# Optimization experiments

Hardware: AMD Instinct MI355X
Metric: run time of the kernel (lower is better)

## Reference

```python
import jax, jax.numpy as jnp
import numpy as np

IN_C, OUT_C, MAX_SIZE = 512, 256, 256
N = MAX_SIZE * MAX_SIZE  # 65536 nodes
E = MAX_SIZE * MAX_SIZE  # 65536 edges (before self loops)
NEG_SLOPE = 0.2


def setup_inputs() -> dict:
    key = jax.random.key(0)
    ks = jax.random.split(key, 12)
    s = 1.0 / np.sqrt(IN_C)
    so = 1.0 / np.sqrt(OUT_C)
    return {
        "x": jax.random.normal(ks[0], (N, IN_C), dtype=jnp.float32),
        "x_mask": jnp.ones((N,), dtype=bool),
        "edge_index": jax.random.randint(ks[1], (2, E), 0, N),
        "edge_mask": jnp.ones((E,), dtype=bool),
        "vaild_mask": jnp.ones((MAX_SIZE, MAX_SIZE), dtype=bool),
        # self-loop Linear
        "W_self": jax.random.uniform(ks[2], (IN_C, OUT_C), jnp.float32, -s, s),
        "b_self": jax.random.uniform(ks[3], (OUT_C,), jnp.float32, -s, s),
        # GATv2Conv params (heads=1)
        "W_l": jax.random.uniform(ks[4], (IN_C, OUT_C), jnp.float32, -s, s),
        "b_l": jnp.zeros((OUT_C,), jnp.float32),
        "W_r": jax.random.uniform(ks[5], (IN_C, OUT_C), jnp.float32, -s, s),
        "b_r": jnp.zeros((OUT_C,), jnp.float32),
        "att": jax.random.uniform(ks[6], (OUT_C,), jnp.float32, -so, so),
        "conv_bias": jnp.zeros((OUT_C,), jnp.float32),
        # sk classifier (out_channels -> 1)
        "W_cls": jax.random.uniform(ks[7], (OUT_C, 1), jnp.float32, -so, so),
        "b_cls": jax.random.uniform(ks[8], (1,), jnp.float32, -so, so),
    }


def _forward(x, edge_index, W_self, b_self, W_l, b_l, W_r, b_r, att,
             conv_bias, W_cls, b_cls):
    n = x.shape[0]
    # PyG GATv2Conv adds self-loops by default
    loops = jnp.arange(n, dtype=edge_index.dtype)
    src = jnp.concatenate([edge_index[0], loops])
    dst = jnp.concatenate([edge_index[1], loops])

    x_l = x @ W_l + b_l  # source-side transform (n, out)
    x_r = x @ W_r + b_r  # target-side transform (n, out)

    # per-edge GATv2 attention logits
    h = jax.nn.leaky_relu(x_l[src] + x_r[dst], NEG_SLOPE)  # (Etot, out)
    e = h @ att  # (Etot,)

    # segment softmax over incoming edges of each target node
    m = jnp.full((n,), -jnp.inf, dtype=e.dtype).at[dst].max(e)
    p = jnp.exp(e - m[dst])
    denom = jax.ops.segment_sum(p, dst, num_segments=n)
    alpha = p / denom[dst]

    x_neigh = jax.ops.segment_sum(alpha[:, None] * x_l[src], dst,
                                  num_segments=n) + conv_bias
    x_out = (x @ W_self + b_self) + x_neigh

    # sinkhorn-style row softmax channel (sk_channel=1, n1=n2=max_size)
    ms = MAX_SIZE
    sk = (x_out @ W_cls + b_cls).reshape(ms, ms)
    sk = jax.nn.softmax(sk, axis=-1)
    x_out = x_out + sk.reshape(-1, 1)
    # n1*n2 == max_size**2, so the padded output equals x_out
    return x_out


def reference(x, x_mask, edge_index, edge_mask, vaild_mask, W_self, b_self,
              W_l, b_l, W_r, b_r, att, conv_bias, W_cls, b_cls):
    # masks are all-True (fully valid case): x_valid = x, edges all kept
    return _forward(x, edge_index, W_self, b_self, W_l, b_l, W_r, b_r, att,
                    conv_bias, W_cls, b_cls)
```

## Files before the change

kernel.cpp:

```cpp
#include <hip/hip_runtime.h>
#include <hip/hip_bf16.h>
#include <stdint.h>

#define NNODE 65536
#define NEDGE 65536
#define ETOT  (NNODE + NEDGE)
#define INC   512
#define OUTC  256
#define NEG_SLOPE 0.2f
#define SLOTCAP 32

typedef __attribute__((ext_vector_type(8))) __bf16 bf16x8;
typedef __attribute__((ext_vector_type(4))) float f32x4;

__device__ __forceinline__ float b2f(unsigned short u) {
  return __uint_as_float(((unsigned int)u) << 16);
}
__device__ __forceinline__ unsigned short f2b(float f) {
  unsigned int u = __float_as_uint(f);
  u += 0x7fffu + ((u >> 16) & 1u);
  return (unsigned short)(u >> 16);
}
__device__ __forceinline__ unsigned int pk2(float lo, float hi) {
  return (unsigned int)f2b(lo) | ((unsigned int)f2b(hi) << 16);
}
__device__ __forceinline__ float lrelu(float v) {
  return v > 0.f ? v : NEG_SLOPE * v;
}

__global__ __launch_bounds__(256) void cvt_x_kernel(const float* __restrict__ x,
                                                    unsigned short* __restrict__ xb,
                                                    int* __restrict__ cnt) {
  if (blockIdx.x < 256) cnt[blockIdx.x * 256 + threadIdx.x] = 0;
  size_t i = ((size_t)blockIdx.x * 256 + threadIdx.x) * 8;
  float4 v0 = *(const float4*)(x + i);
  float4 v1 = *(const float4*)(x + i + 4);
  uint4 o;
  o.x = pk2(v0.x, v0.y);
  o.y = pk2(v0.z, v0.w);
  o.z = pk2(v1.x, v1.y);
  o.w = pk2(v1.z, v1.w);
  *(uint4*)(xb + i) = o;
}

__global__ __launch_bounds__(256) void prep_w_kernel(
    const float* __restrict__ Wl, const float* __restrict__ Wr, const float* __restrict__ Ws,
    const float* __restrict__ bl, const float* __restrict__ br, const float* __restrict__ bs,
    unsigned short* __restrict__ WT, float* __restrict__ bcat) {
  int i = blockIdx.x * 256 + threadIdx.x;
  if (i < 768 * 512) {
    int o = i >> 9, k = i & 511;
    float v;
    if (o < 256)      v = Wl[k * 256 + o];
    else if (o < 512) v = Wr[k * 256 + (o - 256)];
    else              v = Ws[k * 256 + (o - 512)];
    WT[i] = f2b(v);
  }
  if (i < 768) {
    bcat[i] = (i < 256) ? bl[i] : (i < 512 ? br[i - 256] : bs[i - 512]);
  }
}

__global__ __launch_bounds__(512) void gemm_kernel(
    const unsigned short* __restrict__ Xb,
    const unsigned short* __restrict__ WT,
    const float* __restrict__ bcat,
    const float* __restrict__ Wcls,
    unsigned short* __restrict__ xl,
    unsigned short* __restrict__ xr,
    unsigned short* __restrict__ xs,
    float* __restrict__ g,
    float* __restrict__ gs) {
  __shared__ __align__(16) char smem[98304];
  unsigned short* ring = (unsigned short*)smem;

  const int wid = blockIdx.x;
  const int xcd = wid & 7;
  const int local = wid >> 3;
  const int by = local % 3;
  const int rowt = xcd * 32 + local / 3;
  const int rowBase = rowt * 256;
  const int colBase = by * 256;

  const int tid = threadIdx.x;
  const int lane = tid & 63;
  const int w = tid >> 6;
  const int wm = (w >> 2) * 128;
  const int wn = (w & 3) * 64;

  f32x4 acc[8][4] = {};

  auto stageh = [&](int c, int hf) {
    const int kk = c * 32;
    const int buf = c % 3;
    const int q = tid;
    const int sl = q & 3;
    const unsigned short* basep = hf ? (WT + (size_t)colBase * 512) : (Xb + (size_t)rowBase * 512);
    unsigned short* ldst = ring + buf * 16384 + hf * 8192;
#pragma unroll
    for (int l = 0; l < 2; ++l) {
      const int r = l * 128 + (q >> 2);
      const int slot = sl ^ ((r >> 1) & 3);
      const unsigned short* gp = basep + (size_t)r * 512 + kk + slot * 8;
      __builtin_amdgcn_global_load_lds(
          (const __attribute__((address_space(1))) void*)gp,
          (__attribute__((address_space(3))) void*)(ldst + l * 4096 + q * 8), 16, 0, 0);
    }
  };

  stageh(0, 0); stageh(0, 1);
  stageh(1, 0); stageh(1, 1);
  asm volatile("s_waitcnt vmcnt(4)" ::: "memory");
  __builtin_amdgcn_s_barrier();

#pragma unroll
  for (int c = 0; c < 16; ++c) {
    const unsigned short* As = ring + (c % 3) * 16384;
    const unsigned short* Bs = As + 8192;
    const int kq = lane >> 4;
    bf16x8 fa[8], fb[4];

#pragma unroll
    for (int m = 0; m < 4; ++m) {
      const int rA = wm + m * 16 + (lane & 15);
      fa[m] = *(const bf16x8*)&As[rA * 32 + ((kq ^ ((rA >> 1) & 3)) << 3)];
    }
#pragma unroll
    for (int n = 0; n < 4; ++n) {
      const int rB = wn + n * 16 + (lane & 15);
      fb[n] = *(const bf16x8*)&Bs[rB * 32 + ((kq ^ ((rB >> 1) & 3)) << 3)];
    }
    if (c + 2 < 16) stageh(c + 2, 0);
    __builtin_amdgcn_s_barrier();
    asm volatile("s_waitcnt lgkmcnt(0)" ::: "memory");
    __builtin_amdgcn_sched_barrier(0);
    __builtin_amdgcn_s_setprio(1);
#pragma unroll
    for (int m = 0; m < 4; ++m)
#pragma unroll
      for (int n = 0; n < 4; ++n)
        acc[m][n] = __builtin_amdgcn_mfma_f32_16x16x32_bf16(fa[m], fb[n], acc[m][n], 0, 0, 0);
    __builtin_amdgcn_s_setprio(0);
    __builtin_amdgcn_s_barrier();

#pragma unroll
    for (int m = 4; m < 8; ++m) {
      const int rA = wm + m * 16 + (lane & 15);
      fa[m] = *(const bf16x8*)&As[rA * 32 + ((kq ^ ((rA >> 1) & 3)) << 3)];
    }
    if (c + 2 < 16) stageh(c + 2, 1);
    __builtin_amdgcn_s_barrier();
    asm volatile("s_waitcnt lgkmcnt(0)" ::: "memory");
    __builtin_amdgcn_sched_barrier(0);
    __builtin_amdgcn_s_setprio(1);
#pragma unroll
    for (int m = 4; m < 8; ++m)
#pragma unroll
      for (int n = 0; n < 4; ++n)
        acc[m][n] = __builtin_amdgcn_mfma_f32_16x16x32_bf16(fa[m], fb[n], acc[m][n], 0, 0, 0);
    __builtin_amdgcn_s_setprio(0);
    if (c <= 13)      asm volatile("s_waitcnt vmcnt(4)" ::: "memory");
    else if (c == 14) asm volatile("s_waitcnt vmcnt(0)" ::: "memory");
    __builtin_amdgcn_s_barrier();
  }

  {
    unsigned short* dst = (by == 0) ? xl : (by == 1) ? xr : xs;
    const bool doG = (by != 1);
    float* eps = (float*)smem + w * 1088;
    float* gpart = (float*)(smem + 40960);
    float biasn[4], wcn[4];
#pragma unroll
    for (int n = 0; n < 4; ++n) {
      biasn[n] = bcat[colBase + wn + n * 16 + (lane & 15)];
      wcn[n] = Wcls[wn + n * 16 + (lane & 15)];
    }
#pragma unroll
    for (int m = 0; m < 8; ++m) {
      float rp[4] = {0.f, 0.f, 0.f, 0.f};
#pragma unroll
      for (int n = 0; n < 4; ++n)
#pragma unroll
        for (int j = 0; j < 4; ++j) {
          const float v = acc[m][n][j] + biasn[n];
          eps[((lane >> 4) * 4 + j) * 68 + n * 16 + (lane & 15)] = v;
          rp[j] += v * wcn[n];
        }
#pragma unroll
      for (int it = 0; it < 2; ++it) {
        const int r16 = it * 8 + (lane >> 3);
        const int c8 = (lane & 7) * 8;
        const float* srcp = eps + r16 * 68 + c8;
        float4 v0 = *(const float4*)srcp;
        float4 v1 = *(const float4*)(srcp + 4);
        uint4 o;
        o.x = pk2(v0.x, v0.y);
        o.y = pk2(v0.z, v0.w);
        o.z = pk2(v1.x, v1.y);
        o.w = pk2(v1.z, v1.w);
        *(uint4*)(dst + (size_t)(rowBase + wm + m * 16 + r16) * 256 + wn + c8) = o;
      }
      if (doG) {
#pragma unroll
        for (int j = 0; j < 4; ++j) {
          float s = rp[j];
          s += __shfl_xor(s, 1);
          s += __shfl_xor(s, 2);
          s += __shfl_xor(s, 4);
          s += __shfl_xor(s, 8);
          if ((lane & 15) == 0)
            gpart[(wm + m * 16 + (lane >> 4) * 4 + j) * 4 + (w & 3)] = s;
        }
      }
    }
    __syncthreads();
    if (doG && tid < 256) {
      float s = gpart[tid * 4] + gpart[tid * 4 + 1] + gpart[tid * 4 + 2] + gpart[tid * 4 + 3];
      ((by == 0) ? g : gs)[rowBase + tid] = s;
    }
  }
}

__global__ __launch_bounds__(256) void edge_logit_kernel(
    const int* __restrict__ ei,
    const unsigned short* __restrict__ xl,
    const unsigned short* __restrict__ xr,
    const float* __restrict__ att,
    int* __restrict__ cnt,
    int* __restrict__ slot_src,
    float* __restrict__ slot_e) {
  const int j = blockIdx.x * 8 + (threadIdx.x >> 5);
  const int lane = threadIdx.x & 31;
  int src, dst;
  if (j < NEDGE) { src = ei[j]; dst = ei[NEDGE + j]; }
  else           { src = j - NEDGE; dst = src; }
  const int c = lane * 8;
  uint4 ul = *(const uint4*)(xl + (size_t)src * 256 + c);
  uint4 ur = *(const uint4*)(xr + (size_t)dst * 256 + c);
  float4 a0 = *(const float4*)(att + c);
  float4 a1 = *(const float4*)(att + c + 4);
  float s = lrelu(b2f((unsigned short)ul.x) + b2f((unsigned short)ur.x)) * a0.x
          + lrelu(b2f((unsigned short)(ul.x >> 16)) + b2f((unsigned short)(ur.x >> 16))) * a0.y
          + lrelu(b2f((unsigned short)ul.y) + b2f((unsigned short)ur.y)) * a0.z
          + lrelu(b2f((unsigned short)(ul.y >> 16)) + b2f((unsigned short)(ur.y >> 16))) * a0.w
          + lrelu(b2f((unsigned short)ul.z) + b2f((unsigned short)ur.z)) * a1.x
          + lrelu(b2f((unsigned short)(ul.z >> 16)) + b2f((unsigned short)(ur.z >> 16))) * a1.y
          + lrelu(b2f((unsigned short)ul.w) + b2f((unsigned short)ur.w)) * a1.z
          + lrelu(b2f((unsigned short)(ul.w >> 16)) + b2f((unsigned short)(ur.w >> 16))) * a1.w;
#pragma unroll
  for (int off = 16; off; off >>= 1) s += __shfl_xor(s, off);
  if (lane == 0) {
    const int pos = atomicAdd(&cnt[dst], 1);
    if (pos < SLOTCAP) {
      slot_src[dst * SLOTCAP + pos] = src;
      slot_e[dst * SLOTCAP + pos] = s;
    }
  }
}

__global__ __launch_bounds__(256) void logit_kernel(
    const int* __restrict__ cnt,
    const int* __restrict__ slot_src, const float* __restrict__ slot_e,
    const float* __restrict__ g, const float* __restrict__ gs,
    float* __restrict__ logits) {
  const int n = blockIdx.x * 256 + threadIdx.x;
  const int base = n * SLOTCAP;
  const int deg = cnt[n];
  float m = -1e30f;
  for (int k = 0; k < deg; ++k) m = fmaxf(m, slot_e[base + k]);
  float denom = 0.f, wsum = 0.f;
  for (int k = 0; k < deg; ++k) {
    const float p = __expf(slot_e[base + k] - m);
    denom += p;
    wsum += p * g[slot_src[base + k]];
  }
  logits[n] = gs[n] + wsum / denom;
}

__global__ __launch_bounds__(256) void node_sk_kernel(
    const int* __restrict__ cnt,
    const int* __restrict__ slot_src, const float* __restrict__ slot_e,
    const unsigned short* __restrict__ xl,
    const unsigned short* __restrict__ xs,
    const float* __restrict__ conv_bias,
    const float* __restrict__ logits,
    float* __restrict__ out) {
  const int n = blockIdx.x * 4 + (threadIdx.x >> 6);
  const int lane = threadIdx.x & 63;
  const int base = n * SLOTCAP;
  const int deg = cnt[n];

  float m = -1e30f;
  for (int k = 0; k < deg; ++k) m = fmaxf(m, slot_e[base + k]);
  float denom = 0.f;
  for (int k = 0; k < deg; ++k) denom += __expf(slot_e[base + k] - m);
  const float inv = 1.f / denom;

  const int c = lane * 4;
  float4 accv = {0.f, 0.f, 0.f, 0.f};
  for (int k = 0; k < deg; ++k) {
    const float alpha = __expf(slot_e[base + k] - m) * inv;
    const int src = slot_src[base + k];
    ushort4 u = *(const ushort4*)(xl + (size_t)src * 256 + c);
    accv.x += alpha * b2f(u.x);
    accv.y += alpha * b2f(u.y);
    accv.z += alpha * b2f(u.z);
    accv.w += alpha * b2f(u.w);
  }

  const int r = n >> 8;
  float4 lv = *(const float4*)(logits + r * 256 + c);
  float lm = fmaxf(fmaxf(lv.x, lv.y), fmaxf(lv.z, lv.w));
#pragma unroll
  for (int off = 32; off; off >>= 1) lm = fmaxf(lm, __shfl_xor(lm, off));
  float ls = __expf(lv.x - lm) + __expf(lv.y - lm) + __expf(lv.z - lm) + __expf(lv.w - lm);
#pragma unroll
  for (int off = 32; off; off >>= 1) ls += __shfl_xor(ls, off);
  const float softval = __expf(logits[n] - lm) / ls;

  ushort4 s4 = *(const ushort4*)(xs + (size_t)n * 256 + c);
  float4 cb = *(const float4*)(conv_bias + c);
  float4 cur;
  cur.x = b2f(s4.x) + accv.x + cb.x + softval;
  cur.y = b2f(s4.y) + accv.y + cb.y + softval;
  cur.z = b2f(s4.z) + accv.z + cb.z + softval;
  cur.w = b2f(s4.w) + accv.w + cb.w + softval;
  *(float4*)(out + (size_t)n * 256 + c) = cur;
}

extern "C" void kernel_launch(void* const* d_in, const int* in_sizes, int n_in,
                              void* d_out, int out_size, void* d_ws, size_t ws_size,
                              hipStream_t stream) {
  const float* x        = (const float*)d_in[0];
  const int*   ei       = (const int*)d_in[2];
  const float* W_self   = (const float*)d_in[5];
  const float* b_self   = (const float*)d_in[6];
  const float* W_l      = (const float*)d_in[7];
  const float* b_l      = (const float*)d_in[8];
  const float* W_r      = (const float*)d_in[9];
  const float* b_r      = (const float*)d_in[10];
  const float* att      = (const float*)d_in[11];
  const float* conv_bias= (const float*)d_in[12];
  const float* W_cls    = (const float*)d_in[13];
  float* out = (float*)d_out;

  char* ws = (char*)d_ws;
  size_t off = 0;
  auto alloc = [&](size_t bytes) {
    char* p = ws + off;
    off += (bytes + 255) & ~(size_t)255;
    return p;
  };
  unsigned short* xb   = (unsigned short*)alloc((size_t)NNODE * INC * 2);
  unsigned short* WT   = (unsigned short*)alloc((size_t)768 * 512 * 2);
  float*          bcat = (float*)alloc(768 * 4);
  unsigned short* xlb  = (unsigned short*)alloc((size_t)NNODE * OUTC * 2);
  unsigned short* xrb  = (unsigned short*)alloc((size_t)NNODE * OUTC * 2);
  unsigned short* xsb  = (unsigned short*)alloc((size_t)NNODE * OUTC * 2);
  int*            cnt  = (int*)alloc((size_t)NNODE * 4);
  float*          logits  = (float*)alloc((size_t)NNODE * 4);
  float*          gbuf    = (float*)alloc((size_t)NNODE * 4);
  float*          gsbuf   = (float*)alloc((size_t)NNODE * 4);
  int*   slot_src = (int*)xb;
  float* slot_e   = (float*)(xb + (size_t)NNODE * SLOTCAP * 2);
  (void)ws_size; (void)in_sizes; (void)n_in; (void)out_size;

  cvt_x_kernel<<<(NNODE * INC) / (256 * 8), 256, 0, stream>>>(x, xb, cnt);
  prep_w_kernel<<<(768 * 512 + 255) / 256, 256, 0, stream>>>(W_l, W_r, W_self, b_l, b_r, b_self, WT, bcat);
  gemm_kernel<<<768, 512, 0, stream>>>(xb, WT, bcat, W_cls, xlb, xrb, xsb, gbuf, gsbuf);
  edge_logit_kernel<<<ETOT / 8, 256, 0, stream>>>(ei, xlb, xrb, att, cnt, slot_src, slot_e);
  logit_kernel<<<NNODE / 256, 256, 0, stream>>>(cnt, slot_src, slot_e, gbuf, gsbuf, logits);
  node_sk_kernel<<<NNODE / 4, 256, 0, stream>>>(cnt, slot_src, slot_e, xlb, xsb, conv_bias,
                                                logits, out);
}
```

Before: 191.0 us.

## Fuse fp32-to-bf16 conversion of x into GEMM LDS staging

Removes the separate x conversion kernel and has the GEMM stream fp32 x into LDS, converting to bf16 while building MFMA fragments. The counter zeroing moves into the weight prep kernel, and slot buffers get their own workspace. The aim is to avoid writing and re-reading a bf16 copy of x and to drop one launch. In exchange, the GEMM reads twice as many bytes of x per column tile, uses more LDS, and adds conversion ALU work in its inner loop.

```diff
diff --git a/kernel.cpp b/kernel.cpp
--- a/kernel.cpp
+++ b/kernel.cpp
@@ -28,25 +28,10 @@
   return v > 0.f ? v : NEG_SLOPE * v;
 }
 
-__global__ __launch_bounds__(256) void cvt_x_kernel(const float* __restrict__ x,
-                                                    unsigned short* __restrict__ xb,
-                                                    int* __restrict__ cnt) {
-  if (blockIdx.x < 256) cnt[blockIdx.x * 256 + threadIdx.x] = 0;
-  size_t i = ((size_t)blockIdx.x * 256 + threadIdx.x) * 8;
-  float4 v0 = *(const float4*)(x + i);
-  float4 v1 = *(const float4*)(x + i + 4);
-  uint4 o;
-  o.x = pk2(v0.x, v0.y);
-  o.y = pk2(v0.z, v0.w);
-  o.z = pk2(v1.x, v1.y);
-  o.w = pk2(v1.z, v1.w);
-  *(uint4*)(xb + i) = o;
-}
-
 __global__ __launch_bounds__(256) void prep_w_kernel(
     const float* __restrict__ Wl, const float* __restrict__ Wr, const float* __restrict__ Ws,
     const float* __restrict__ bl, const float* __restrict__ br, const float* __restrict__ bs,
-    unsigned short* __restrict__ WT, float* __restrict__ bcat) {
+    unsigned short* __restrict__ WT, float* __restrict__ bcat, int* __restrict__ cnt) {
   int i = blockIdx.x * 256 + threadIdx.x;
   if (i < 768 * 512) {
     int o = i >> 9, k = i & 511;
@@ -56,13 +41,14 @@
     else              v = Ws[k * 256 + (o - 512)];
     WT[i] = f2b(v);
   }
+  if (i < NNODE) cnt[i] = 0;
   if (i < 768) {
     bcat[i] = (i < 256) ? bl[i] : (i < 512 ? br[i - 256] : bs[i - 512]);
   }
 }
 
 __global__ __launch_bounds__(512) void gemm_kernel(
-    const unsigned short* __restrict__ Xb,
+    const float* __restrict__ Xf,
     const unsigned short* __restrict__ WT,
     const float* __restrict__ bcat,
     const float* __restrict__ Wcls,
@@ -71,8 +57,7 @@
     unsigned short* __restrict__ xs,
     float* __restrict__ g,
     float* __restrict__ gs) {
-  __shared__ __align__(16) char smem[98304];
-  unsigned short* ring = (unsigned short*)smem;
+  __shared__ __align__(16) char smem[147456];
 
   const int wid = blockIdx.x;
   const int xcd = wid & 7;
@@ -90,47 +75,67 @@
 
   f32x4 acc[8][4] = {};
 
-  auto stageh = [&](int c, int hf) {
+  auto stageA = [&](int c) {
     const int kk = c * 32;
-    const int buf = c % 3;
+    float* abase = (float*)(smem + (c % 3) * 49152);
+    const int q = tid;
+#pragma unroll
+    for (int l = 0; l < 4; ++l) {
+      const int r = l * 64 + (q >> 3);
+      const int slot = (q & 7) ^ (r & 7);
+      const float* gp = Xf + (size_t)(rowBase + r) * 512 + kk + slot * 4;
+      __builtin_amdgcn_global_load_lds(
+          (const __attribute__((address_space(1))) void*)gp,
+          (__attribute__((address_space(3))) void*)(abase + l * 2048 + q * 4), 16, 0, 0);
+    }
+  };
+  auto stageB = [&](int c) {
+    const int kk = c * 32;
+    unsigned short* bbase = (unsigned short*)(smem + (c % 3) * 49152 + 32768);
     const int q = tid;
     const int sl = q & 3;
-    const unsigned short* basep = hf ? (WT + (size_t)colBase * 512) : (Xb + (size_t)rowBase * 512);
-    unsigned short* ldst = ring + buf * 16384 + hf * 8192;
 #pragma unroll
     for (int l = 0; l < 2; ++l) {
       const int r = l * 128 + (q >> 2);
       const int slot = sl ^ ((r >> 1) & 3);
-      const unsigned short* gp = basep + (size_t)r * 512 + kk + slot * 8;
+      const unsigned short* gp = WT + (size_t)(colBase + r) * 512 + kk + slot * 8;
       __builtin_amdgcn_global_load_lds(
           (const __attribute__((address_space(1))) void*)gp,
-          (__attribute__((address_space(3))) void*)(ldst + l * 4096 + q * 8), 16, 0, 0);
+          (__attribute__((address_space(3))) void*)(bbase + l * 4096 + q * 8), 16, 0, 0);
     }
   };
 
-  stageh(0, 0); stageh(0, 1);
-  stageh(1, 0); stageh(1, 1);
-  asm volatile("s_waitcnt vmcnt(4)" ::: "memory");
+  stageA(0); stageB(0);
+  stageA(1); stageB(1);
+  asm volatile("s_waitcnt vmcnt(6)" ::: "memory");
   __builtin_amdgcn_s_barrier();
 
 #pragma unroll
   for (int c = 0; c < 16; ++c) {
-    const unsigned short* As = ring + (c % 3) * 16384;
-    const unsigned short* Bs = As + 8192;
+    const float* Af = (const float*)(smem + (c % 3) * 49152);
+    const unsigned short* Bs = (const unsigned short*)(smem + (c % 3) * 49152 + 32768);
     const int kq = lane >> 4;
     bf16x8 fa[8], fb[4];
 
-#pragma unroll
-    for (int m = 0; m < 4; ++m) {
-      const int rA = wm + m * 16 + (lane & 15);
-      fa[m] = *(const bf16x8*)&As[rA * 32 + ((kq ^ ((rA >> 1) & 3)) << 3)];
-    }
+#define LDA(mi) { \
+      const int rA = wm + (mi) * 16 + (lane & 15); \
+      const int s0 = (2 * kq) ^ (rA & 7); \
+      const int s1 = (2 * kq + 1) ^ (rA & 7); \
+      float4 v0 = *(const float4*)&Af[rA * 32 + s0 * 4]; \
+      float4 v1 = *(const float4*)&Af[rA * 32 + s1 * 4]; \
+      union { uint4 u; bf16x8 v; } cv; \
+      cv.u.x = pk2(v0.x, v0.y); cv.u.y = pk2(v0.z, v0.w); \
+      cv.u.z = pk2(v1.x, v1.y); cv.u.w = pk2(v1.z, v1.w); \
+      fa[mi] = cv.v; \
+    }
+
+    LDA(0) LDA(1) LDA(2) LDA(3)
 #pragma unroll
     for (int n = 0; n < 4; ++n) {
       const int rB = wn + n * 16 + (lane & 15);
       fb[n] = *(const bf16x8*)&Bs[rB * 32 + ((kq ^ ((rB >> 1) & 3)) << 3)];
     }
-    if (c + 2 < 16) stageh(c + 2, 0);
+    if (c + 2 < 16) stageA(c + 2);
     __builtin_amdgcn_s_barrier();
     asm volatile("s_waitcnt lgkmcnt(0)" ::: "memory");
     __builtin_amdgcn_sched_barrier(0);
@@ -143,12 +148,9 @@
     __builtin_amdgcn_s_setprio(0);
     __builtin_amdgcn_s_barrier();
 
-#pragma unroll
-    for (int m = 4; m < 8; ++m) {
-      const int rA = wm + m * 16 + (lane & 15);
-      fa[m] = *(const bf16x8*)&As[rA * 32 + ((kq ^ ((rA >> 1) & 3)) << 3)];
-    }
-    if (c + 2 < 16) stageh(c + 2, 1);
+    LDA(4) LDA(5) LDA(6) LDA(7)
+#undef LDA
+    if (c + 2 < 16) stageB(c + 2);
     __builtin_amdgcn_s_barrier();
     asm volatile("s_waitcnt lgkmcnt(0)" ::: "memory");
     __builtin_amdgcn_sched_barrier(0);
@@ -159,7 +161,7 @@
       for (int n = 0; n < 4; ++n)
         acc[m][n] = __builtin_amdgcn_mfma_f32_16x16x32_bf16(fa[m], fb[n], acc[m][n], 0, 0, 0);
     __builtin_amdgcn_s_setprio(0);
-    if (c <= 13)      asm volatile("s_waitcnt vmcnt(4)" ::: "memory");
+    if (c <= 13)      asm volatile("s_waitcnt vmcnt(6)" ::: "memory");
     else if (c == 14) asm volatile("s_waitcnt vmcnt(0)" ::: "memory");
     __builtin_amdgcn_s_barrier();
   }
@@ -351,7 +353,6 @@
     off += (bytes + 255) & ~(size_t)255;
     return p;
   };
-  unsigned short* xb   = (unsigned short*)alloc((size_t)NNODE * INC * 2);
   unsigned short* WT   = (unsigned short*)alloc((size_t)768 * 512 * 2);
   float*          bcat = (float*)alloc(768 * 4);
   unsigned short* xlb  = (unsigned short*)alloc((size_t)NNODE * OUTC * 2);
@@ -361,13 +362,13 @@
   float*          logits  = (float*)alloc((size_t)NNODE * 4);
   float*          gbuf    = (float*)alloc((size_t)NNODE * 4);
   float*          gsbuf   = (float*)alloc((size_t)NNODE * 4);
-  int*   slot_src = (int*)xb;
-  float* slot_e   = (float*)(xb + (size_t)NNODE * SLOTCAP * 2);
+  int*   slot_src = (int*)alloc((size_t)NNODE * SLOTCAP * 4);
+  float* slot_e   = (float*)alloc((size_t)NNODE * SLOTCAP * 4);
   (void)ws_size; (void)in_sizes; (void)n_in; (void)out_size;
 
-  cvt_x_kernel<<<(NNODE * INC) / (256 * 8), 256, 0, stream>>>(x, xb, cnt);
-  prep_w_kernel<<<(768 * 512 + 255) / 256, 256, 0, stream>>>(W_l, W_r, W_self, b_l, b_r, b_self, WT, bcat);
-  gemm_kernel<<<768, 512, 0, stream>>>(xb, WT, bcat, W_cls, xlb, xrb, xsb, gbuf, gsbuf);
+  prep_w_kernel<<<(768 * 512 + 255) / 256, 256, 0, stream>>>(W_l, W_r, W_self, b_l, b_r, b_self,
+                                                             WT, bcat, cnt);
+  gemm_kernel<<<768, 512, 0, stream>>>(x, WT, bcat, W_cls, xlb, xrb, xsb, gbuf, gsbuf);
   edge_logit_kernel<<<ETOT / 8, 256, 0, stream>>>(ei, xlb, xrb, att, cnt, slot_src, slot_e);
   logit_kernel<<<NNODE / 256, 256, 0, stream>>>(cnt, slot_src, slot_e, gbuf, gsbuf, logits);
   node_sk_kernel<<<NNODE / 4, 256, 0, stream>>>(cnt, slot_src, slot_e, xlb, xsb, conv_bias,
```

Result: slower. 223.0 us (+16.7%).

## Merge prep kernels and switch GEMM to double-buffered LDS pipeline

Applied to the files above, without the earlier changes.

Fuses the x-conversion and weight-transpose kernels into one launch to save a kernel launch. The GEMM drops its 3-stage ring and split half-step schedule in favour of a simpler 2-buffer scheme: it prefetches the next k-chunk, then does all 8x4 MFMAs per step with a full vmcnt(0) wait and a barrier. LDS use falls from 96KB to 64KB and launch_bounds asks for more occupancy. The cost is less latency hiding per block, since every iteration waits for its global loads to finish.

```diff
diff --git a/kernel.cpp b/kernel.cpp
--- a/kernel.cpp
+++ b/kernel.cpp
@@ -28,11 +28,13 @@
   return v > 0.f ? v : NEG_SLOPE * v;
 }
 
-__global__ __launch_bounds__(256) void cvt_x_kernel(const float* __restrict__ x,
-                                                    unsigned short* __restrict__ xb,
-                                                    int* __restrict__ cnt) {
-  if (blockIdx.x < 256) cnt[blockIdx.x * 256 + threadIdx.x] = 0;
-  size_t i = ((size_t)blockIdx.x * 256 + threadIdx.x) * 8;
+__global__ __launch_bounds__(256) void prep_kernel(
+    const float* __restrict__ x, unsigned short* __restrict__ xb, int* __restrict__ cnt,
+    const float* __restrict__ Wl, const float* __restrict__ Wr, const float* __restrict__ Ws,
+    const float* __restrict__ bl, const float* __restrict__ br, const float* __restrict__ bs,
+    unsigned short* __restrict__ WT, float* __restrict__ bcat) {
+  const int b = blockIdx.x, t = threadIdx.x;
+  size_t i = ((size_t)b * 256 + t) * 8;
   float4 v0 = *(const float4*)(x + i);
   float4 v1 = *(const float4*)(x + i + 4);
   uint4 o;
@@ -41,27 +43,22 @@
   o.z = pk2(v1.x, v1.y);
   o.w = pk2(v1.z, v1.w);
   *(uint4*)(xb + i) = o;
-}
-
-__global__ __launch_bounds__(256) void prep_w_kernel(
-    const float* __restrict__ Wl, const float* __restrict__ Wr, const float* __restrict__ Ws,
-    const float* __restrict__ bl, const float* __restrict__ br, const float* __restrict__ bs,
-    unsigned short* __restrict__ WT, float* __restrict__ bcat) {
-  int i = blockIdx.x * 256 + threadIdx.x;
-  if (i < 768 * 512) {
-    int o = i >> 9, k = i & 511;
+  if (b < 256) cnt[b * 256 + t] = 0;
+  const int wi = b * 256 + t;
+  if (wi < 768 * 512) {
+    const int oc = wi >> 9, k = wi & 511;
     float v;
-    if (o < 256)      v = Wl[k * 256 + o];
-    else if (o < 512) v = Wr[k * 256 + (o - 256)];
-    else              v = Ws[k * 256 + (o - 512)];
-    WT[i] = f2b(v);
-  }
-  if (i < 768) {
-    bcat[i] = (i < 256) ? bl[i] : (i < 512 ? br[i - 256] : bs[i - 512]);
-  }
-}
-
-__global__ __launch_bounds__(512) void gemm_kernel(
+    if (oc < 256)      v = Wl[k * 256 + oc];
+    else if (oc < 512) v = Wr[k * 256 + (oc - 256)];
+    else               v = Ws[k * 256 + (oc - 512)];
+    WT[wi] = f2b(v);
+  }
+  if (wi < 768) {
+    bcat[wi] = (wi < 256) ? bl[wi] : (wi < 512 ? br[wi - 256] : bs[wi - 512]);
+  }
+}
+
+__global__ __launch_bounds__(512, 4) void gemm_kernel(
     const unsigned short* __restrict__ Xb,
     const unsigned short* __restrict__ WT,
     const float* __restrict__ bcat,
@@ -71,7 +68,7 @@
     unsigned short* __restrict__ xs,
     float* __restrict__ g,
     float* __restrict__ gs) {
-  __shared__ __align__(16) char smem[98304];
+  __shared__ __align__(16) char smem[65536];
   unsigned short* ring = (unsigned short*)smem;
 
   const int wid = blockIdx.x;
@@ -92,7 +89,7 @@
 
   auto stageh = [&](int c, int hf) {
     const int kk = c * 32;
-    const int buf = c % 3;
+    const int buf = c & 1;
     const int q = tid;
     const int sl = q & 3;
     const unsigned short* basep = hf ? (WT + (size_t)colBase * 512) : (Xb + (size_t)rowBase * 512);
@@ -109,19 +106,21 @@
   };
 
   stageh(0, 0); stageh(0, 1);
-  stageh(1, 0); stageh(1, 1);
-  asm volatile("s_waitcnt vmcnt(4)" ::: "memory");
+  asm volatile("s_waitcnt vmcnt(0)" ::: "memory");
   __builtin_amdgcn_s_barrier();
+  __builtin_amdgcn_sched_barrier(0);
 
 #pragma unroll
   for (int c = 0; c < 16; ++c) {
-    const unsigned short* As = ring + (c % 3) * 16384;
+    const unsigned short* As = ring + (c & 1) * 16384;
     const unsigned short* Bs = As + 8192;
     const int kq = lane >> 4;
     bf16x8 fa[8], fb[4];
 
-#pragma unroll
-    for (int m = 0; m < 4; ++m) {
+    if (c + 1 < 16) { stageh(c + 1, 0); stageh(c + 1, 1); }
+
+#pragma unroll
+    for (int m = 0; m < 8; ++m) {
       const int rA = wm + m * 16 + (lane & 15);
       fa[m] = *(const bf16x8*)&As[rA * 32 + ((kq ^ ((rA >> 1) & 3)) << 3)];
     }
@@ -130,38 +129,18 @@
       const int rB = wn + n * 16 + (lane & 15);
       fb[n] = *(const bf16x8*)&Bs[rB * 32 + ((kq ^ ((rB >> 1) & 3)) << 3)];
     }
-    if (c + 2 < 16) stageh(c + 2, 0);
-    __builtin_amdgcn_s_barrier();
     asm volatile("s_waitcnt lgkmcnt(0)" ::: "memory");
     __builtin_amdgcn_sched_barrier(0);
     __builtin_amdgcn_s_setprio(1);
 #pragma unroll
-    for (int m = 0; m < 4; ++m)
+    for (int m = 0; m < 8; ++m)
 #pragma unroll
       for (int n = 0; n < 4; ++n)
         acc[m][n] = __builtin_amdgcn_mfma_f32_16x16x32_bf16(fa[m], fb[n], acc[m][n], 0, 0, 0);
     __builtin_amdgcn_s_setprio(0);
+    asm volatile("s_waitcnt vmcnt(0)" ::: "memory");
     __builtin_amdgcn_s_barrier();
-
-#pragma unroll
-    for (int m = 4; m < 8; ++m) {
-      const int rA = wm + m * 16 + (lane & 15);
-      fa[m] = *(const bf16x8*)&As[rA * 32 + ((kq ^ ((rA >> 1) & 3)) << 3)];
-    }
-    if (c + 2 < 16) stageh(c + 2, 1);
-    __builtin_amdgcn_s_barrier();
-    asm volatile("s_waitcnt lgkmcnt(0)" ::: "memory");
     __builtin_amdgcn_sched_barrier(0);
-    __builtin_amdgcn_s_setprio(1);
-#pragma unroll
-    for (int m = 4; m < 8; ++m)
-#pragma unroll
-      for (int n = 0; n < 4; ++n)
-        acc[m][n] = __builtin_amdgcn_mfma_f32_16x16x32_bf16(fa[m], fb[n], acc[m][n], 0, 0, 0);
-    __builtin_amdgcn_s_setprio(0);
-    if (c <= 13)      asm volatile("s_waitcnt vmcnt(4)" ::: "memory");
-    else if (c == 14) asm volatile("s_waitcnt vmcnt(0)" ::: "memory");
-    __builtin_amdgcn_s_barrier();
   }
 
   {
@@ -365,8 +344,9 @@
   float* slot_e   = (float*)(xb + (size_t)NNODE * SLOTCAP * 2);
   (void)ws_size; (void)in_sizes; (void)n_in; (void)out_size;
 
-  cvt_x_kernel<<<(NNODE * INC) / (256 * 8), 256, 0, stream>>>(x, xb, cnt);
-  prep_w_kernel<<<(768 * 512 + 255) / 256, 256, 0, stream>>>(W_l, W_r, W_self, b_l, b_r, b_self, WT, bcat);
+  prep_kernel<<<(NNODE * INC) / (256 * 8), 256, 0, stream>>>(x, xb, cnt,
+                                                             W_l, W_r, W_self, b_l, b_r, b_self,
+                                                             WT, bcat);
   gemm_kernel<<<768, 512, 0, stream>>>(xb, WT, bcat, W_cls, xlb, xrb, xsb, gbuf, gsbuf);
   edge_logit_kernel<<<ETOT / 8, 256, 0, stream>>>(ei, xlb, xrb, att, cnt, slot_src, slot_e);
   logit_kernel<<<NNODE / 256, 256, 0, stream>>>(cnt, slot_src, slot_e, gbuf, gsbuf, logits);
```

After: 762.3 us. 3.99x slower.
